# Optimization experiments

Measured on AMD Instinct MI355X. Metric: run time of the kernel, lower is better.

Reference implementation:

```python
import jax, jax.numpy as jnp
import numpy as np

K = 5  # number of nearest neighbors (module default)


def setup_inputs() -> dict:
    key = jax.random.key(0)
    k1, k2 = jax.random.split(key)
    source_pc = jax.random.normal(k1, (2, 8192, 3), dtype=jnp.float32)
    target_pc = jax.random.normal(k2, (2, 8192, 3), dtype=jnp.float32)
    return {"source_pc": source_pc, "target_pc": target_pc}


def _valid_mask(pc_flat):
    # point is valid if any coordinate is nonzero (move_zero_point)
    return jnp.any(pc_flat != 0.0, axis=-1)


def reference(source_pc, target_pc):
    # move_zero_point flattens all batches into one batch-1 cloud; we emulate
    # the filtering with masks (invalid targets -> +inf distance, invalid
    # sources excluded from the mean) to stay jit-compatible.
    src = source_pc.reshape(-1, 3)   # [Ms, 3] query points
    tgt = target_pc.reshape(-1, 3)   # [Nt, 3] reference points
    src_mask = _valid_mask(src)      # [Ms]
    tgt_mask = _valid_mask(tgt)      # [Nt]

    # squared pairwise distances: |s|^2 + |t|^2 - 2 s.t  -> [Ms, Nt]
    s2 = jnp.sum(src * src, axis=-1)[:, None]
    t2 = jnp.sum(tgt * tgt, axis=-1)[None, :]
    d2 = s2 + t2 - 2.0 * jnp.einsum('md,nd->mn', src, tgt)
    d = jnp.sqrt(jnp.maximum(d2, 1e-12))

    BIG = jnp.float32(1e10)
    d = jnp.where(tgt_mask[None, :], d, BIG)  # drop zero target points

    # k smallest distances per source point (knn returns Euclidean dists)
    neg_topk, _ = jax.lax.top_k(-d, K)        # [Ms, K]
    knn_d = -neg_topk

    # mean over valid source points only
    w = src_mask.astype(knn_d.dtype)
    total = jnp.sum(knn_d * w[:, None])
    count = jnp.sum(w) * K
    return total / count
```

## Files before the change

kernel.cpp:

```cpp
#include <hip/hip_runtime.h>
#include <math.h>

#define KNN 5
#define BLOCK 256
#define TILE_T 2048
#define WAVES_PER_BLOCK (BLOCK / 64)
#define SRC_PER_WAVE 4
#define SRC_PER_BLOCK (WAVES_PER_BLOCK * SRC_PER_WAVE)


__device__ __forceinline__ float vmin(float a, float b) {
    float r;
    asm("v_min_f32 %0, %1, %2" : "=v"(r) : "v"(a), "v"(b));
    return r;
}
__device__ __forceinline__ float vmax(float a, float b) {
    float r;
    asm("v_max_f32 %0, %1, %2" : "=v"(r) : "v"(a), "v"(b));
    return r;
}


__global__ void init_acc_kernel(float* acc) {
    acc[0] = 0.0f;
    acc[1] = 0.0f;
}

__global__ void finalize_kernel(const float* acc, float* out) {
    out[0] = acc[0] / (acc[1] * (float)KNN);
}

#define INS5(K0, K1, K2, K3, K4, V)                                       \
    do {                                                                  \
        float _v = (V);                                                   \
        K4 = __builtin_amdgcn_fmed3f(K3, K4, _v);                         \
        K3 = __builtin_amdgcn_fmed3f(K2, K3, _v);                         \
        K2 = __builtin_amdgcn_fmed3f(K1, K2, _v);                         \
        K1 = __builtin_amdgcn_fmed3f(K0, K1, _v);                         \
        K0 = vmin(K0, _v);                                                \
    } while (0)


__global__ __launch_bounds__(BLOCK) void knn_kernel(
        const float* __restrict__ src, const float* __restrict__ tgt,
        float* __restrict__ acc, int ms, int nt) {
    __shared__ __align__(16) float xs[TILE_T];
    __shared__ __align__(16) float ys[TILE_T];
    __shared__ __align__(16) float zs[TILE_T];
    __shared__ __align__(16) float w2[TILE_T];
    __shared__ float red_s[WAVES_PER_BLOCK];
    __shared__ float red_c[WAVES_PER_BLOCK];

    const int tid = threadIdx.x;
    const int wv = tid >> 6;
    const int lane = tid & 63;
    const int sbase = (blockIdx.x * WAVES_PER_BLOCK + wv) * SRC_PER_WAVE;

    float nx[SRC_PER_WAVE], ny[SRC_PER_WAVE], nz[SRC_PER_WAVE];
    float s2a[SRC_PER_WAVE], svalid[SRC_PER_WAVE];
#pragma unroll
    for (int s = 0; s < SRC_PER_WAVE; ++s) {
        int sp = sbase + s;
        float x = 0.0f, y = 0.0f, z = 0.0f;
        if (sp < ms) {
            x = src[3 * sp + 0];
            y = src[3 * sp + 1];
            z = src[3 * sp + 2];
        }
        svalid[s] = (sp < ms && (x != 0.0f || y != 0.0f || z != 0.0f)) ? 1.0f : 0.0f;
        nx[s] = -2.0f * x;
        ny[s] = -2.0f * y;
        nz[s] = -2.0f * z;
        s2a[s] = fmaf(x, x, fmaf(y, y, z * z));
    }

    float q0[SRC_PER_WAVE], q1[SRC_PER_WAVE], q2[SRC_PER_WAVE],
          q3[SRC_PER_WAVE], q4[SRC_PER_WAVE];
#pragma unroll
    for (int s = 0; s < SRC_PER_WAVE; ++s) {
        q0[s] = 1e30f; q1[s] = 1e30f; q2[s] = 1e30f; q3[s] = 1e30f; q4[s] = 1e30f;
    }

    for (int t0 = 0; t0 < nt; t0 += TILE_T) {
        if (t0 + TILE_T <= nt) {
            const float4* t4 = reinterpret_cast<const float4*>(tgt + (size_t)t0 * 3);
#pragma unroll
            for (int cc = 0; cc < TILE_T / 4; cc += BLOCK) {
                int c = cc + tid;
                float4 f0 = t4[3 * c + 0];
                float4 f1 = t4[3 * c + 1];
                float4 f2 = t4[3 * c + 2];
                float px[4] = {f0.x, f0.w, f1.z, f2.y};
                float py[4] = {f0.y, f1.x, f1.w, f2.z};
                float pz[4] = {f0.z, f1.y, f2.x, f2.w};
                float pw[4];
#pragma unroll
                for (int j = 0; j < 4; ++j) {
                    bool v = (px[j] != 0.0f) || (py[j] != 0.0f) || (pz[j] != 0.0f);
                    if (!v) { px[j] = 1e10f; py[j] = 0.0f; pz[j] = 0.0f; }
                    pw[j] = fmaf(px[j], px[j], fmaf(py[j], py[j], pz[j] * pz[j]));
                }
                int t = 4 * c;
                *reinterpret_cast<float4*>(&xs[t]) = make_float4(px[0], px[1], px[2], px[3]);
                *reinterpret_cast<float4*>(&ys[t]) = make_float4(py[0], py[1], py[2], py[3]);
                *reinterpret_cast<float4*>(&zs[t]) = make_float4(pz[0], pz[1], pz[2], pz[3]);
                *reinterpret_cast<float4*>(&w2[t]) = make_float4(pw[0], pw[1], pw[2], pw[3]);
            }
        } else {
            int cnt = nt - t0;
            for (int t = tid; t < TILE_T; t += BLOCK) {
                float x = 1e10f, y = 0.0f, z = 0.0f;
                if (t < cnt) {
                    x = tgt[3 * (size_t)(t0 + t) + 0];
                    y = tgt[3 * (size_t)(t0 + t) + 1];
                    z = tgt[3 * (size_t)(t0 + t) + 2];
                    if (x == 0.0f && y == 0.0f && z == 0.0f) { x = 1e10f; y = 0.0f; z = 0.0f; }
                }
                xs[t] = x; ys[t] = y; zs[t] = z;
                w2[t] = fmaf(x, x, fmaf(y, y, z * z));
            }
        }
        __syncthreads();

#pragma unroll 2
        for (int i = 0; i < TILE_T / 256; ++i) {
            int t = (i << 8) + (lane << 2);
            float4 x4 = *reinterpret_cast<const float4*>(&xs[t]);
            float4 y4 = *reinterpret_cast<const float4*>(&ys[t]);
            float4 z4 = *reinterpret_cast<const float4*>(&zs[t]);
            float4 w4 = *reinterpret_cast<const float4*>(&w2[t]);
#pragma unroll
            for (int s = 0; s < SRC_PER_WAVE; ++s) {
                float qa = fmaf(nx[s], x4.x, fmaf(ny[s], y4.x, fmaf(nz[s], z4.x, w4.x)));
                float qb = fmaf(nx[s], x4.y, fmaf(ny[s], y4.y, fmaf(nz[s], z4.y, w4.y)));
                float qc = fmaf(nx[s], x4.z, fmaf(ny[s], y4.z, fmaf(nz[s], z4.z, w4.z)));
                float qd = fmaf(nx[s], x4.w, fmaf(ny[s], y4.w, fmaf(nz[s], z4.w, w4.w)));
                INS5(q0[s], q1[s], q2[s], q3[s], q4[s], qa);
                INS5(q0[s], q1[s], q2[s], q3[s], q4[s], qb);
                INS5(q0[s], q1[s], q2[s], q3[s], q4[s], qc);
                INS5(q0[s], q1[s], q2[s], q3[s], q4[s], qd);
            }
        }
        __syncthreads();
    }

#pragma unroll
    for (int off = 32; off >= 1; off >>= 1) {
#pragma unroll
        for (int s = 0; s < SRC_PER_WAVE; ++s) {
            float a0 = q0[s], a1 = q1[s], a2 = q2[s], a3 = q3[s], a4 = q4[s];
            float b0 = __shfl_xor(a0, off);
            float b1 = __shfl_xor(a1, off);
            float b2 = __shfl_xor(a2, off);
            float b3 = __shfl_xor(a3, off);
            float b4 = __shfl_xor(a4, off);
            q0[s] = vmin(a0, b0);
            q1[s] = vmin(vmin(a1, b1), vmax(a0, b0));
            q2[s] = vmin(vmin(a2, b2), vmin(vmax(a0, b1), vmax(a1, b0)));
            q3[s] = vmin(vmin(a3, b3),
                         vmin(vmax(a0, b2), vmin(vmax(a1, b1), vmax(a2, b0))));
            q4[s] = vmin(vmin(a4, b4),
                         vmin(vmin(vmax(a0, b3), vmax(a1, b2)),
                              vmin(vmax(a2, b1), vmax(a3, b0))));
        }
    }

    if (lane == 0) {
        float ssum = 0.0f, scnt = 0.0f;
#pragma unroll
        for (int s = 0; s < SRC_PER_WAVE; ++s) {
            float d0 = sqrtf(fmaxf(q0[s] + s2a[s], 1e-12f));
            float d1 = sqrtf(fmaxf(q1[s] + s2a[s], 1e-12f));
            float d2 = sqrtf(fmaxf(q2[s] + s2a[s], 1e-12f));
            float d3 = sqrtf(fmaxf(q3[s] + s2a[s], 1e-12f));
            float d4 = sqrtf(fmaxf(q4[s] + s2a[s], 1e-12f));
            ssum += svalid[s] * (d0 + d1 + d2 + d3 + d4);
            scnt += svalid[s];
        }
        red_s[wv] = ssum;
        red_c[wv] = scnt;
    }
    __syncthreads();

    if (tid == 0) {
        float s = 0.0f, c = 0.0f;
#pragma unroll
        for (int i = 0; i < WAVES_PER_BLOCK; ++i) {
            s += red_s[i];
            c += red_c[i];
        }
        atomicAdd(&acc[0], s);
        atomicAdd(&acc[1], c);
    }
}


extern "C" void kernel_launch(void* const* d_in, const int* in_sizes, int n_in,
                              void* d_out, int out_size, void* d_ws, size_t ws_size,
                              hipStream_t stream) {
    const float* src = (const float*)d_in[0];
    const float* tgt = (const float*)d_in[1];
    const int ms = in_sizes[0] / 3;
    const int nt = in_sizes[1] / 3;

    float* acc = (float*)d_ws;
    init_acc_kernel<<<1, 1, 0, stream>>>(acc);

    const int blocks = (ms + SRC_PER_BLOCK - 1) / SRC_PER_BLOCK;
    knn_kernel<<<blocks, BLOCK, 0, stream>>>(src, tgt, acc, ms, nt);

    finalize_kernel<<<1, 1, 0, stream>>>(acc, (float*)d_out);
}
```

Before: 82.18 us.

## Split target range across two grid halves and merge partial top-5 lists

The KNN kernel now handles 8 sources per wave instead of 4 and splits the target cloud into two halves along grid.y. Each half writes per-source partial top-5 lists to workspace, and a new merge kernel combines them, computes the distances and does the reduction. Doubling sources per wave reuses each shared-memory target load across more sources, and the split keeps the block count up. The cost is an extra kernel launch, workspace traffic and higher register pressure. A fallback mono kernel runs when the workspace is too small.

New measurement: 80.28 us. 1.02x faster.

```diff
diff --git a/kernel.cpp b/kernel.cpp
--- a/kernel.cpp
+++ b/kernel.cpp
@@ -5,9 +5,9 @@
 #define BLOCK 256
 #define TILE_T 2048
 #define WAVES_PER_BLOCK (BLOCK / 64)
-#define SRC_PER_WAVE 4
-#define SRC_PER_BLOCK (WAVES_PER_BLOCK * SRC_PER_WAVE)
-
+#define SRCW 8
+#define SRC_PER_BLOCK (WAVES_PER_BLOCK * SRCW)
+#define NSPLIT 2
 
 __device__ __forceinline__ float vmin(float a, float b) {
     float r;
@@ -18,16 +18,6 @@
     float r;
     asm("v_max_f32 %0, %1, %2" : "=v"(r) : "v"(a), "v"(b));
     return r;
-}
-
-
-__global__ void init_acc_kernel(float* acc) {
-    acc[0] = 0.0f;
-    acc[1] = 0.0f;
-}
-
-__global__ void finalize_kernel(const float* acc, float* out) {
-    out[0] = acc[0] / (acc[1] * (float)KNN);
 }
 
 #define INS5(K0, K1, K2, K3, K4, V)                                       \
@@ -40,26 +30,49 @@
         K0 = vmin(K0, _v);                                                \
     } while (0)
 
-
-__global__ __launch_bounds__(BLOCK) void knn_kernel(
+#define MERGE55(a0, a1, a2, a3, a4, b0, b1, b2, b3, b4)                   \
+    do {                                                                  \
+        float r0 = vmin(a0, b0);                                          \
+        float r1 = vmin(vmin(a1, b1), vmax(a0, b0));                      \
+        float r2 = vmin(vmin(a2, b2), vmin(vmax(a0, b1), vmax(a1, b0)));  \
+        float r3 = vmin(vmin(a3, b3),                                     \
+                        vmin(vmax(a0, b2), vmin(vmax(a1, b1), vmax(a2, b0)))); \
+        float r4 = vmin(vmin(a4, b4),                                     \
+                        vmin(vmin(vmax(a0, b3), vmax(a1, b2)),            \
+                             vmin(vmax(a2, b1), vmax(a3, b0))));          \
+        a0 = r0; a1 = r1; a2 = r2; a3 = r3; a4 = r4;                      \
+    } while (0)
+
+
+__global__ void init_acc_kernel(float* acc) {
+    acc[0] = 0.0f;
+    acc[1] = 0.0f;
+}
+
+__global__ void finalize_kernel(const float* acc, float* out) {
+    out[0] = acc[0] / (acc[1] * (float)KNN);
+}
+
+
+__global__ __launch_bounds__(BLOCK, 4) void knn_split_kernel(
         const float* __restrict__ src, const float* __restrict__ tgt,
-        float* __restrict__ acc, int ms, int nt) {
+        float* __restrict__ partials, int ms, int nt, int nth, int spad) {
     __shared__ __align__(16) float xs[TILE_T];
     __shared__ __align__(16) float ys[TILE_T];
     __shared__ __align__(16) float zs[TILE_T];
     __shared__ __align__(16) float w2[TILE_T];
-    __shared__ float red_s[WAVES_PER_BLOCK];
-    __shared__ float red_c[WAVES_PER_BLOCK];
 
     const int tid = threadIdx.x;
     const int wv = tid >> 6;
     const int lane = tid & 63;
-    const int sbase = (blockIdx.x * WAVES_PER_BLOCK + wv) * SRC_PER_WAVE;
-
-    float nx[SRC_PER_WAVE], ny[SRC_PER_WAVE], nz[SRC_PER_WAVE];
-    float s2a[SRC_PER_WAVE], svalid[SRC_PER_WAVE];
-#pragma unroll
-    for (int s = 0; s < SRC_PER_WAVE; ++s) {
+    const int sbase = (blockIdx.x * WAVES_PER_BLOCK + wv) * SRCW;
+    const int half = blockIdx.y;
+    const int hbase = half * nth;
+    const int hend = min(nt, hbase + nth);
+
+    float nx[SRCW], ny[SRCW], nz[SRCW];
+#pragma unroll
+    for (int s = 0; s < SRCW; ++s) {
         int sp = sbase + s;
         float x = 0.0f, y = 0.0f, z = 0.0f;
         if (sp < ms) {
@@ -67,26 +80,23 @@
             y = src[3 * sp + 1];
             z = src[3 * sp + 2];
         }
-        svalid[s] = (sp < ms && (x != 0.0f || y != 0.0f || z != 0.0f)) ? 1.0f : 0.0f;
         nx[s] = -2.0f * x;
         ny[s] = -2.0f * y;
         nz[s] = -2.0f * z;
-        s2a[s] = fmaf(x, x, fmaf(y, y, z * z));
-    }
-
-    float q0[SRC_PER_WAVE], q1[SRC_PER_WAVE], q2[SRC_PER_WAVE],
-          q3[SRC_PER_WAVE], q4[SRC_PER_WAVE];
-#pragma unroll
-    for (int s = 0; s < SRC_PER_WAVE; ++s) {
+    }
+
+    float q0[SRCW], q1[SRCW], q2[SRCW], q3[SRCW], q4[SRCW];
+#pragma unroll
+    for (int s = 0; s < SRCW; ++s) {
         q0[s] = 1e30f; q1[s] = 1e30f; q2[s] = 1e30f; q3[s] = 1e30f; q4[s] = 1e30f;
     }
 
-    for (int t0 = 0; t0 < nt; t0 += TILE_T) {
-        if (t0 + TILE_T <= nt) {
-            const float4* t4 = reinterpret_cast<const float4*>(tgt + (size_t)t0 * 3);
+    for (int t0 = hbase; t0 < hend; t0 += TILE_T) {
+        if (t0 + TILE_T <= hend) {
 #pragma unroll
             for (int cc = 0; cc < TILE_T / 4; cc += BLOCK) {
                 int c = cc + tid;
+                const float4* t4 = reinterpret_cast<const float4*>(tgt + (size_t)t0 * 3);
                 float4 f0 = t4[3 * c + 0];
                 float4 f1 = t4[3 * c + 1];
                 float4 f2 = t4[3 * c + 2];
@@ -107,7 +117,7 @@
                 *reinterpret_cast<float4*>(&w2[t]) = make_float4(pw[0], pw[1], pw[2], pw[3]);
             }
         } else {
-            int cnt = nt - t0;
+            int cnt = hend - t0;
             for (int t = tid; t < TILE_T; t += BLOCK) {
                 float x = 1e10f, y = 0.0f, z = 0.0f;
                 if (t < cnt) {
@@ -130,7 +140,7 @@
             float4 z4 = *reinterpret_cast<const float4*>(&zs[t]);
             float4 w4 = *reinterpret_cast<const float4*>(&w2[t]);
 #pragma unroll
-            for (int s = 0; s < SRC_PER_WAVE; ++s) {
+            for (int s = 0; s < SRCW; ++s) {
                 float qa = fmaf(nx[s], x4.x, fmaf(ny[s], y4.x, fmaf(nz[s], z4.x, w4.x)));
                 float qb = fmaf(nx[s], x4.y, fmaf(ny[s], y4.y, fmaf(nz[s], z4.y, w4.y)));
                 float qc = fmaf(nx[s], x4.z, fmaf(ny[s], y4.z, fmaf(nz[s], z4.z, w4.z)));
@@ -147,28 +157,167 @@
 #pragma unroll
     for (int off = 32; off >= 1; off >>= 1) {
 #pragma unroll
-        for (int s = 0; s < SRC_PER_WAVE; ++s) {
-            float a0 = q0[s], a1 = q1[s], a2 = q2[s], a3 = q3[s], a4 = q4[s];
-            float b0 = __shfl_xor(a0, off);
-            float b1 = __shfl_xor(a1, off);
-            float b2 = __shfl_xor(a2, off);
-            float b3 = __shfl_xor(a3, off);
-            float b4 = __shfl_xor(a4, off);
-            q0[s] = vmin(a0, b0);
-            q1[s] = vmin(vmin(a1, b1), vmax(a0, b0));
-            q2[s] = vmin(vmin(a2, b2), vmin(vmax(a0, b1), vmax(a1, b0)));
-            q3[s] = vmin(vmin(a3, b3),
-                         vmin(vmax(a0, b2), vmin(vmax(a1, b1), vmax(a2, b0))));
-            q4[s] = vmin(vmin(a4, b4),
-                         vmin(vmin(vmax(a0, b3), vmax(a1, b2)),
-                              vmin(vmax(a2, b1), vmax(a3, b0))));
-        }
-    }
-
+        for (int s = 0; s < SRCW; ++s) {
+            float b0 = __shfl_xor(q0[s], off);
+            float b1 = __shfl_xor(q1[s], off);
+            float b2 = __shfl_xor(q2[s], off);
+            float b3 = __shfl_xor(q3[s], off);
+            float b4 = __shfl_xor(q4[s], off);
+            MERGE55(q0[s], q1[s], q2[s], q3[s], q4[s], b0, b1, b2, b3, b4);
+        }
+    }
+
+    if (lane == 0) {
+        float* base = partials + ((size_t)half * spad + sbase) * 8;
+#pragma unroll
+        for (int s = 0; s < SRCW; ++s) {
+            if (sbase + s < ms) {
+                *reinterpret_cast<float4*>(base + 8 * s) =
+                    make_float4(q0[s], q1[s], q2[s], q3[s]);
+                *reinterpret_cast<float4*>(base + 8 * s + 4) =
+                    make_float4(q4[s], 0.0f, 0.0f, 0.0f);
+            }
+        }
+    }
+}
+
+
+__global__ __launch_bounds__(BLOCK) void merge_kernel(
+        const float* __restrict__ src, const float* __restrict__ partials,
+        float* __restrict__ acc, int ms, int spad) {
+    __shared__ float red_s[WAVES_PER_BLOCK];
+    __shared__ float red_c[WAVES_PER_BLOCK];
+
+    const int tid = threadIdx.x;
+    const int sp = blockIdx.x * BLOCK + tid;
+
+    float ssum = 0.0f, scnt = 0.0f;
+    if (sp < ms) {
+        const float* r0p = partials + (size_t)sp * 8;
+        const float* r1p = partials + ((size_t)spad + sp) * 8;
+        float4 lo0 = *reinterpret_cast<const float4*>(r0p);
+        float a4 = r0p[4];
+        float4 lo1 = *reinterpret_cast<const float4*>(r1p);
+        float b4 = r1p[4];
+        float a0 = lo0.x, a1 = lo0.y, a2 = lo0.z, a3 = lo0.w;
+        MERGE55(a0, a1, a2, a3, a4, lo1.x, lo1.y, lo1.z, lo1.w, b4);
+
+        float x = src[3 * sp + 0];
+        float y = src[3 * sp + 1];
+        float z = src[3 * sp + 2];
+        bool valid = (x != 0.0f) || (y != 0.0f) || (z != 0.0f);
+        float s2 = fmaf(x, x, fmaf(y, y, z * z));
+        if (valid) {
+            ssum = sqrtf(fmaxf(a0 + s2, 1e-12f)) + sqrtf(fmaxf(a1 + s2, 1e-12f)) +
+                   sqrtf(fmaxf(a2 + s2, 1e-12f)) + sqrtf(fmaxf(a3 + s2, 1e-12f)) +
+                   sqrtf(fmaxf(a4 + s2, 1e-12f));
+            scnt = 1.0f;
+        }
+    }
+
+#pragma unroll
+    for (int off = 32; off >= 1; off >>= 1) {
+        ssum += __shfl_down(ssum, off);
+        scnt += __shfl_down(scnt, off);
+    }
+    if ((tid & 63) == 0) {
+        red_s[tid >> 6] = ssum;
+        red_c[tid >> 6] = scnt;
+    }
+    __syncthreads();
+    if (tid == 0) {
+        float s = 0.0f, c = 0.0f;
+#pragma unroll
+        for (int i = 0; i < WAVES_PER_BLOCK; ++i) { s += red_s[i]; c += red_c[i]; }
+        atomicAdd(&acc[0], s);
+        atomicAdd(&acc[1], c);
+    }
+}
+
+
+__global__ __launch_bounds__(BLOCK) void knn_mono_kernel(
+        const float* __restrict__ src, const float* __restrict__ tgt,
+        float* __restrict__ acc, int ms, int nt) {
+    __shared__ __align__(16) float xs[TILE_T];
+    __shared__ __align__(16) float ys[TILE_T];
+    __shared__ __align__(16) float zs[TILE_T];
+    __shared__ __align__(16) float w2[TILE_T];
+    __shared__ float red_s[WAVES_PER_BLOCK];
+    __shared__ float red_c[WAVES_PER_BLOCK];
+
+    const int tid = threadIdx.x;
+    const int wv = tid >> 6;
+    const int lane = tid & 63;
+    const int sbase = (blockIdx.x * WAVES_PER_BLOCK + wv) * 4;
+
+    float nx[4], ny[4], nz[4], s2a[4], svalid[4];
+#pragma unroll
+    for (int s = 0; s < 4; ++s) {
+        int sp = sbase + s;
+        float x = 0.0f, y = 0.0f, z = 0.0f;
+        if (sp < ms) {
+            x = src[3 * sp + 0]; y = src[3 * sp + 1]; z = src[3 * sp + 2];
+        }
+        svalid[s] = (sp < ms && (x != 0.0f || y != 0.0f || z != 0.0f)) ? 1.0f : 0.0f;
+        nx[s] = -2.0f * x; ny[s] = -2.0f * y; nz[s] = -2.0f * z;
+        s2a[s] = fmaf(x, x, fmaf(y, y, z * z));
+    }
+    float q0[4], q1[4], q2[4], q3[4], q4[4];
+#pragma unroll
+    for (int s = 0; s < 4; ++s) {
+        q0[s] = 1e30f; q1[s] = 1e30f; q2[s] = 1e30f; q3[s] = 1e30f; q4[s] = 1e30f;
+    }
+    for (int t0 = 0; t0 < nt; t0 += TILE_T) {
+        int cnt = min(TILE_T, nt - t0);
+        for (int t = tid; t < TILE_T; t += BLOCK) {
+            float x = 1e10f, y = 0.0f, z = 0.0f;
+            if (t < cnt) {
+                x = tgt[3 * (size_t)(t0 + t) + 0];
+                y = tgt[3 * (size_t)(t0 + t) + 1];
+                z = tgt[3 * (size_t)(t0 + t) + 2];
+                if (x == 0.0f && y == 0.0f && z == 0.0f) { x = 1e10f; y = 0.0f; z = 0.0f; }
+            }
+            xs[t] = x; ys[t] = y; zs[t] = z;
+            w2[t] = fmaf(x, x, fmaf(y, y, z * z));
+        }
+        __syncthreads();
+#pragma unroll 2
+        for (int i = 0; i < TILE_T / 256; ++i) {
+            int t = (i << 8) + (lane << 2);
+            float4 x4 = *reinterpret_cast<const float4*>(&xs[t]);
+            float4 y4 = *reinterpret_cast<const float4*>(&ys[t]);
+            float4 z4 = *reinterpret_cast<const float4*>(&zs[t]);
+            float4 w4 = *reinterpret_cast<const float4*>(&w2[t]);
+#pragma unroll
+            for (int s = 0; s < 4; ++s) {
+                float qa = fmaf(nx[s], x4.x, fmaf(ny[s], y4.x, fmaf(nz[s], z4.x, w4.x)));
+                float qb = fmaf(nx[s], x4.y, fmaf(ny[s], y4.y, fmaf(nz[s], z4.y, w4.y)));
+                float qc = fmaf(nx[s], x4.z, fmaf(ny[s], y4.z, fmaf(nz[s], z4.z, w4.z)));
+                float qd = fmaf(nx[s], x4.w, fmaf(ny[s], y4.w, fmaf(nz[s], z4.w, w4.w)));
+                INS5(q0[s], q1[s], q2[s], q3[s], q4[s], qa);
+                INS5(q0[s], q1[s], q2[s], q3[s], q4[s], qb);
+                INS5(q0[s], q1[s], q2[s], q3[s], q4[s], qc);
+                INS5(q0[s], q1[s], q2[s], q3[s], q4[s], qd);
+            }
+        }
+        __syncthreads();
+    }
+#pragma unroll
+    for (int off = 32; off >= 1; off >>= 1) {
+#pragma unroll
+        for (int s = 0; s < 4; ++s) {
+            float b0 = __shfl_xor(q0[s], off);
+            float b1 = __shfl_xor(q1[s], off);
+            float b2 = __shfl_xor(q2[s], off);
+            float b3 = __shfl_xor(q3[s], off);
+            float b4 = __shfl_xor(q4[s], off);
+            MERGE55(q0[s], q1[s], q2[s], q3[s], q4[s], b0, b1, b2, b3, b4);
+        }
+    }
     if (lane == 0) {
         float ssum = 0.0f, scnt = 0.0f;
 #pragma unroll
-        for (int s = 0; s < SRC_PER_WAVE; ++s) {
+        for (int s = 0; s < 4; ++s) {
             float d0 = sqrtf(fmaxf(q0[s] + s2a[s], 1e-12f));
             float d1 = sqrtf(fmaxf(q1[s] + s2a[s], 1e-12f));
             float d2 = sqrtf(fmaxf(q2[s] + s2a[s], 1e-12f));
@@ -181,14 +330,10 @@
         red_c[wv] = scnt;
     }
     __syncthreads();
-
     if (tid == 0) {
         float s = 0.0f, c = 0.0f;
 #pragma unroll
-        for (int i = 0; i < WAVES_PER_BLOCK; ++i) {
-            s += red_s[i];
-            c += red_c[i];
-        }
+        for (int i = 0; i < WAVES_PER_BLOCK; ++i) { s += red_s[i]; c += red_c[i]; }
         atomicAdd(&acc[0], s);
         atomicAdd(&acc[1], c);
     }
@@ -206,8 +351,22 @@
     float* acc = (float*)d_ws;
     init_acc_kernel<<<1, 1, 0, stream>>>(acc);
 
-    const int blocks = (ms + SRC_PER_BLOCK - 1) / SRC_PER_BLOCK;
-    knn_kernel<<<blocks, BLOCK, 0, stream>>>(src, tgt, acc, ms, nt);
+    const int ngroups = (ms + SRC_PER_BLOCK - 1) / SRC_PER_BLOCK;
+    const int spad = ngroups * SRC_PER_BLOCK;
+    int nth = (nt + NSPLIT - 1) / NSPLIT;
+    nth = (nth + TILE_T - 1) / TILE_T * TILE_T;
+
+    const size_t need = 16 + (size_t)NSPLIT * spad * 8 * sizeof(float);
+
+    if (ws_size >= need) {
+        float* partials = (float*)((char*)d_ws + 16);
+        dim3 grid(ngroups, NSPLIT);
+        knn_split_kernel<<<grid, BLOCK, 0, stream>>>(src, tgt, partials, ms, nt, nth, spad);
+        merge_kernel<<<(ms + BLOCK - 1) / BLOCK, BLOCK, 0, stream>>>(src, partials, acc, ms, spad);
+    } else {
+        const int blocks = (ms + 15) / 16;
+        knn_mono_kernel<<<blocks, BLOCK, 0, stream>>>(src, tgt, acc, ms, nt);
+    }
 
     finalize_kernel<<<1, 1, 0, stream>>>(acc, (float*)d_out);
 }
```
